# Performance work log

Hardware: AMD Instinct MI355X
Metric: run time of the kernel (lower is better)

## Reference

```python
import jax, jax.numpy as jnp
import numpy as np

U, I, D, E = 100000, 50000, 128, 3200000


def setup_inputs() -> dict:
    key = jax.random.key(0)
    k0, k1, k2, k3, k4 = jax.random.split(key, 5)
    stdv = 1.0 / np.sqrt(D)
    return {
        "user_embedding": jax.random.uniform(k0, (U, D), jnp.float32, -stdv, stdv),
        "item_embedding": jax.random.uniform(k1, (I, D), jnp.float32, -stdv, stdv),
        "edge_vals": jax.random.uniform(k2, (E,), jnp.float32),  # normalized adj values
        "edge_u": jax.random.randint(k3, (E,), 0, U, jnp.int32),
        "edge_i": jax.random.randint(k4, (E,), 0, I, jnp.int32),
        "n_layers": 3,
    }


def reference(user_embedding, item_embedding, edge_vals, edge_u, edge_i, n_layers):
    # LightGCN forward: alternate SpMM on bipartite graph G [U,I] (COO edges),
    # then average embeddings across layers 0..n_layers.
    num_users = user_embedding.shape[0]
    num_items = item_embedding.shape[0]
    u_list = [user_embedding]
    i_list = [item_embedding]
    w = edge_vals[:, None]  # [E,1]
    for layer in range(n_layers):
        # u_{l+1} = G @ i_l : gather item rows along edges, scale, scatter-add to users
        new_u = jax.ops.segment_sum(w * i_list[layer][edge_i], edge_u,
                                    num_segments=num_users)
        # i_{l+1} = G^T @ u_l
        new_i = jax.ops.segment_sum(w * u_list[layer][edge_u], edge_i,
                                    num_segments=num_items)
        u_list.append(new_u)
        i_list.append(new_i)
    denom = jnp.float32(n_layers + 1)
    embed_user = sum(u_list) / denom
    embed_item = sum(i_list) / denom
    return (embed_user, embed_item)
```

## Files before the change

### kernel.cpp

```cpp
#include <hip/hip_runtime.h>


#define D 128
#define CHUNK 16384
#define SRCMASK 0x3FFFF
#define TPB 256

__device__ inline unsigned pack4(float a, float b, float c, float d, float qs) {
    int q0 = __float2int_rn(a * qs), q1 = __float2int_rn(b * qs);
    int q2 = __float2int_rn(c * qs), q3 = __float2int_rn(d * qs);
    return ((unsigned)(q0 & 255)) | ((unsigned)(q1 & 255) << 8) |
           ((unsigned)(q2 & 255) << 16) | ((unsigned)(q3 & 255) << 24);
}

__device__ inline void acc_q8(float4& sa, float4& sb, uint2 raw, float m) {
    unsigned x = raw.x, y = raw.y;
    sa.x += m * (float)((int)(x << 24) >> 24);
    sa.y += m * (float)((int)(x << 16) >> 24);
    sa.z += m * (float)((int)(x <<  8) >> 24);
    sa.w += m * (float)((int)(x      ) >> 24);
    sb.x += m * (float)((int)(y << 24) >> 24);
    sb.y += m * (float)((int)(y << 16) >> 24);
    sb.z += m * (float)((int)(y <<  8) >> 24);
    sb.w += m * (float)((int)(y      ) >> 24);
}

__global__ __launch_bounds__(TPB) void k_quant8(
    const float* __restrict__ ue, const float* __restrict__ ie,
    uint2* __restrict__ h0q, float* __restrict__ sc0, int U, int UA, int NP) {
    int row = blockIdx.x * (TPB / 16) + (threadIdx.x >> 4);
    if (row >= NP) return;
    int lane = threadIdx.x & 15;
    float4 a = make_float4(0.f, 0.f, 0.f, 0.f);
    float4 b = make_float4(0.f, 0.f, 0.f, 0.f);
    const float* p = nullptr;
    if (row < U)        p = ue + (size_t)row * D + lane * 8;
    else if (row >= UA) p = ie + (size_t)(row - UA) * D + lane * 8;
    if (p) { a = *(const float4*)p; b = *(const float4*)(p + 4); }
    float m = fmaxf(fmaxf(fmaxf(fabsf(a.x), fabsf(a.y)), fmaxf(fabsf(a.z), fabsf(a.w))),
                    fmaxf(fmaxf(fabsf(b.x), fabsf(b.y)), fmaxf(fabsf(b.z), fabsf(b.w))));
    for (int d_ = 1; d_ < 16; d_ <<= 1) m = fmaxf(m, __shfl_xor(m, d_));
    float qs = (m > 0.f) ? 127.f / m : 0.f;
    uint2 q;
    q.x = pack4(a.x, a.y, a.z, a.w, qs);
    q.y = pack4(b.x, b.y, b.z, b.w, qs);
    h0q[(size_t)row * 16 + lane] = q;
    if (lane == 0) sc0[row] = m * (1.f / 127.f);
}

__global__ __launch_bounds__(256) void k_count(const int* __restrict__ eu,
                                               const int* __restrict__ ei,
                                               int* __restrict__ C, int E, int NB, int UA) {
    extern __shared__ int hist[];
    for (int k = threadIdx.x; k < NB; k += blockDim.x) hist[k] = 0;
    __syncthreads();
    int base = blockIdx.x * CHUNK;
    int n = min(CHUNK, E - base);
    for (int t = threadIdx.x; t < n; t += blockDim.x) {
        int u = eu[base + t];
        int i = ei[base + t];
        atomicAdd(&hist[u >> 6], 1);
        atomicAdd(&hist[(UA + i) >> 6], 1);
    }
    __syncthreads();
    int* Crow = C + (size_t)blockIdx.x * NB;
    for (int k = threadIdx.x; k < NB; k += blockDim.x) Crow[k] = hist[k];
}

__global__ void k_btot(const int* __restrict__ C, int* __restrict__ T, int NB, int NC) {
    int b = blockIdx.x * blockDim.x + threadIdx.x;
    if (b >= NB) return;
    int s = 0;
    for (int c = 0; c < NC; ++c) s += C[(size_t)c * NB + b];
    T[b] = s;
}

__global__ __launch_bounds__(1024) void k_scan(const int* __restrict__ T,
                                               int* __restrict__ offb, int N) {
    __shared__ int partial[1024];
    int t = threadIdx.x;
    int CH = (N + 1023) >> 10;
    int c0 = min(t * CH, N), c1 = min(c0 + CH, N);
    int sum = 0;
    for (int k = c0; k < c1; ++k) sum += T[k];
    partial[t] = sum;
    __syncthreads();
    for (int s = 1; s < 1024; s <<= 1) {
        int add = (t >= s) ? partial[t - s] : 0;
        __syncthreads();
        partial[t] += add;
        __syncthreads();
    }
    int run = (t == 0) ? 0 : partial[t - 1];
    for (int k = c0; k < c1; ++k) { offb[k] = run; run += T[k]; }
    if (t == 0) offb[N] = partial[1023];
}

__global__ void k_colscan(const int* __restrict__ C, const int* __restrict__ offb,
                          int* __restrict__ colScan, int NB, int NC) {
    int b = blockIdx.x * blockDim.x + threadIdx.x;
    if (b >= NB) return;
    int run = offb[b];
    for (int c = 0; c < NC; ++c) {
        size_t k = (size_t)c * NB + b;
        colScan[k] = run;
        run += C[k];
    }
}

__global__ __launch_bounds__(256) void k_cscatter(
    const int* __restrict__ eu, const int* __restrict__ ei, const float* __restrict__ w,
    const int* __restrict__ colScan, uint2* __restrict__ entA, int E, int NB, int UA) {
    extern __shared__ int cursor[];
    int c = blockIdx.x, t = threadIdx.x;
    const int* cs = colScan + (size_t)c * NB;
    for (int k = t; k < NB; k += 256) cursor[k] = cs[k];
    __syncthreads();
    int base = c * CHUNK;
    int n = min(CHUNK, E - base);
    for (int k = t; k < n; k += 256) {
        int u = eu[base + k];
        int gi = UA + ei[base + k];
        unsigned wb = __float_as_uint(w[base + k]);
        int pA = atomicAdd(&cursor[u >> 6], 1);
        entA[pA] = make_uint2(((unsigned)(u & 63) << 18) | (unsigned)gi, wb);
        int pB = atomicAdd(&cursor[gi >> 6], 1);
        entA[pB] = make_uint2(((unsigned)(gi & 63) << 18) | (unsigned)u, wb);
    }
}

__global__ __launch_bounds__(256) void k_rowsort(
    const uint2* __restrict__ entA, uint2* __restrict__ entB,
    const int* __restrict__ offb, int* __restrict__ off, int NP) {
    __shared__ int hist[64];
    __shared__ int rowOff[64];
    __shared__ int cursor[64];
    int b = blockIdx.x, t = threadIdx.x;
    int segBase = offb[b];
    int len = offb[b + 1] - segBase;
    if (t < 64) hist[t] = 0;
    __syncthreads();
    for (int k = t; k < len; k += 256)
        atomicAdd(&hist[entA[segBase + k].x >> 18], 1);
    __syncthreads();
    if (t == 0) {
        int run = 0;
        for (int r = 0; r < 64; ++r) { rowOff[r] = run; cursor[r] = run; run += hist[r]; }
    }
    __syncthreads();
    for (int k = t; k < len; k += 256) {
        uint2 e = entA[segBase + k];
        int p = atomicAdd(&cursor[e.x >> 18], 1);
        entB[segBase + p] = e;
    }
    if (t < 64) {
        int g = b * 64 + t;
        if (g <= NP) off[g] = segBase + rowOff[t];
    }
}

template <int MODE>
__global__ __launch_bounds__(TPB) void k_spmm(
    const uint2* __restrict__ q, const float* __restrict__ sc,
    uint2* __restrict__ nxtq, float* __restrict__ scn,
    const uint2* __restrict__ e1q, const float* __restrict__ sc1,
    const uint2* __restrict__ e2q, const float* __restrict__ sc2,
    const float* __restrict__ ue, const float* __restrict__ ie,
    float* __restrict__ out,
    const int* __restrict__ off, const uint2* __restrict__ csr,
    int U, int UA, int NP) {
    int row = blockIdx.x * (TPB / 16) + (threadIdx.x >> 4);
    if (row >= NP) return;
    int lane = threadIdx.x & 15;
    int beg = off[row], end = off[row + 1];
    float4 sa = make_float4(0.f, 0.f, 0.f, 0.f);
    float4 sb = make_float4(0.f, 0.f, 0.f, 0.f);

    int nIter = (end - beg) >> 2;
    int p = beg;
    if (nIter > 0) {
        uint2 m0 = csr[p], m1 = csr[p + 1], m2 = csr[p + 2], m3 = csr[p + 3];
        for (int it = 0; it < nIter; ++it) {
            int s0 = m0.x & SRCMASK, s1 = m1.x & SRCMASK;
            int s2 = m2.x & SRCMASK, s3 = m3.x & SRCMASK;
            uint2 g0 = q[(size_t)s0 * 16 + lane];
            uint2 g1 = q[(size_t)s1 * 16 + lane];
            uint2 g2 = q[(size_t)s2 * 16 + lane];
            uint2 g3 = q[(size_t)s3 * 16 + lane];
            float f0 = __uint_as_float(m0.y) * sc[s0];
            float f1 = __uint_as_float(m1.y) * sc[s1];
            float f2 = __uint_as_float(m2.y) * sc[s2];
            float f3 = __uint_as_float(m3.y) * sc[s3];
            int pn = p + 4;
            if (it + 1 < nIter) {
                m0 = csr[pn]; m1 = csr[pn + 1]; m2 = csr[pn + 2]; m3 = csr[pn + 3];
            }
            acc_q8(sa, sb, g0, f0);
            acc_q8(sa, sb, g1, f1);
            acc_q8(sa, sb, g2, f2);
            acc_q8(sa, sb, g3, f3);
            p = pn;
        }
    }
    for (; p < end; ++p) {
        uint2 m_ = csr[p];
        int s_ = m_.x & SRCMASK;
        uint2 g_ = q[(size_t)s_ * 16 + lane];
        acc_q8(sa, sb, g_, __uint_as_float(m_.y) * sc[s_]);
    }

    if (MODE == 0) {
        float m = fmaxf(fmaxf(fmaxf(fabsf(sa.x), fabsf(sa.y)), fmaxf(fabsf(sa.z), fabsf(sa.w))),
                        fmaxf(fmaxf(fabsf(sb.x), fabsf(sb.y)), fmaxf(fabsf(sb.z), fabsf(sb.w))));
        for (int d_ = 1; d_ < 16; d_ <<= 1) m = fmaxf(m, __shfl_xor(m, d_));
        float qs = (m > 0.f) ? 127.f / m : 0.f;
        uint2 qo;
        qo.x = pack4(sa.x, sa.y, sa.z, sa.w, qs);
        qo.y = pack4(sb.x, sb.y, sb.z, sb.w, qs);
        nxtq[(size_t)row * 16 + lane] = qo;
        if (lane == 0) scn[row] = m * (1.f / 127.f);
    } else {
        int outRow;
        const float* e0p;
        if (row < U)        { outRow = row;            e0p = ue + (size_t)row * D + lane * 8; }
        else if (row >= UA) { outRow = U + (row - UA); e0p = ie + (size_t)(row - UA) * D + lane * 8; }
        else return;
        float4 e0a = *(const float4*)e0p;
        float4 e0b = *(const float4*)(e0p + 4);
        uint2 q1 = e1q[(size_t)row * 16 + lane]; float s1r = sc1[row];
        uint2 q2 = e2q[(size_t)row * 16 + lane]; float s2r = sc2[row];
        unsigned x1 = q1.x, y1 = q1.y, x2 = q2.x, y2 = q2.y;
        float4 ra, rb;
        ra.x = 0.25f * (e0a.x + s1r * (float)((int)(x1 << 24) >> 24) + s2r * (float)((int)(x2 << 24) >> 24) + sa.x);
        ra.y = 0.25f * (e0a.y + s1r * (float)((int)(x1 << 16) >> 24) + s2r * (float)((int)(x2 << 16) >> 24) + sa.y);
        ra.z = 0.25f * (e0a.z + s1r * (float)((int)(x1 <<  8) >> 24) + s2r * (float)((int)(x2 <<  8) >> 24) + sa.z);
        ra.w = 0.25f * (e0a.w + s1r * (float)((int)(x1      ) >> 24) + s2r * (float)((int)(x2      ) >> 24) + sa.w);
        rb.x = 0.25f * (e0b.x + s1r * (float)((int)(y1 << 24) >> 24) + s2r * (float)((int)(y2 << 24) >> 24) + sb.x);
        rb.y = 0.25f * (e0b.y + s1r * (float)((int)(y1 << 16) >> 24) + s2r * (float)((int)(y2 << 16) >> 24) + sb.y);
        rb.z = 0.25f * (e0b.z + s1r * (float)((int)(y1 <<  8) >> 24) + s2r * (float)((int)(y2 <<  8) >> 24) + sb.z);
        rb.w = 0.25f * (e0b.w + s1r * (float)((int)(y1      ) >> 24) + s2r * (float)((int)(y2      ) >> 24) + sb.w);
        float* op = out + (size_t)outRow * D + lane * 8;
        *(float4*)op = ra;
        *(float4*)(op + 4) = rb;
    }
}

extern "C" void kernel_launch(void* const* d_in, const int* in_sizes, int n_in,
                              void* d_out, int out_size, void* d_ws, size_t ws_size,
                              hipStream_t stream) {
    const float* ue = (const float*)d_in[0];
    const float* ie = (const float*)d_in[1];
    const float* w  = (const float*)d_in[2];
    const int*   eu = (const int*)d_in[3];
    const int*   ei = (const int*)d_in[4];

    const int U  = in_sizes[0] / D;
    const int I  = in_sizes[1] / D;
    const int E  = in_sizes[2];
    const int UA = ((U + 63) >> 6) << 6;
    const int NP = UA + I;
    const int NB = (NP + 63) >> 6;
    const int NC = (E + CHUNK - 1) / CHUNK;
    const size_t nE2 = (size_t)2 * E;

    uint2* h0q = (uint2*)d_ws;
    uint2* e1q = h0q + (size_t)NP * 16;
    uint2* e2q = e1q + (size_t)NP * 16;
    float* sc0 = (float*)(e2q + (size_t)NP * 16);
    float* sc1 = sc0 + NP;
    float* sc2 = sc1 + NP;
    uint2* entB = (uint2*)(sc2 + NP);
    int* C       = (int*)(entB + nE2);
    int* colScan = C + (size_t)NC * NB;
    int* T       = colScan + (size_t)NC * NB;
    int* offb    = T + NB;
    int* off     = offb + NB + 1;
    char* tail   = (char*)(off + NP + 1);
    tail += (8 - ((uintptr_t)tail & 7)) & 7;
    uint2* entA  = (uint2*)tail;

    const size_t needed = (size_t)NP * D * 3 + (size_t)NP * 12
                        + nE2 * 8 * 2
                        + ((size_t)2 * NC * NB + NB + (NB + 1) + (NP + 1)) * 4 + 8;
    if (ws_size < needed) return;

    const int nbR = (NP + 15) / 16;

    k_quant8<<<nbR, TPB, 0, stream>>>(ue, ie, h0q, sc0, U, UA, NP);
    k_count<<<NC, 256, (size_t)NB * 4, stream>>>(eu, ei, C, E, NB, UA);
    k_btot<<<(NB + 255) / 256, 256, 0, stream>>>(C, T, NB, NC);
    k_scan<<<1, 1024, 0, stream>>>(T, offb, NB);
    k_colscan<<<(NB + 255) / 256, 256, 0, stream>>>(C, offb, colScan, NB, NC);
    k_cscatter<<<NC, 256, (size_t)NB * 4, stream>>>(eu, ei, w, colScan, entA, E, NB, UA);
    k_rowsort<<<NB, 256, 0, stream>>>(entA, entB, offb, off, NP);

    k_spmm<0><<<nbR, TPB, 0, stream>>>(h0q, sc0, e1q, sc1,
                                       nullptr, nullptr, nullptr, nullptr,
                                       ue, ie, nullptr, off, entB, U, UA, NP);
    k_spmm<0><<<nbR, TPB, 0, stream>>>(e1q, sc1, e2q, sc2,
                                       nullptr, nullptr, nullptr, nullptr,
                                       ue, ie, nullptr, off, entB, U, UA, NP);
    k_spmm<1><<<nbR, TPB, 0, stream>>>(e2q, sc2, nullptr, nullptr,
                                       e1q, sc1, e2q, sc2,
                                       ue, ie, (float*)d_out, off, entB, U, UA, NP);
}
```

Baseline: 646.4 us.

## Tile column scans, shrink edge chunks, widen blocks, and use nontemporal memory ops

The edge chunk size drops from 16384 to 4096, giving more blocks for counting and scatter. The serial per-bucket column sum and column scan are replaced by a two-level tiled scan (k_tile_sum, k_super, then a tiled colscan) so that work spreads over a 2D grid. The preprocessing kernels move to 512 threads per block, and many loads and stores across all kernels become nontemporal to avoid polluting the cache. The risks are a larger histogram matrix (four times the chunks, so C and colScan each grow fourfold) and possible cache-policy penalties on data that is reused, such as csr entries in the later SpMM layers.

```diff
diff --git a/kernel.cpp b/kernel.cpp
--- a/kernel.cpp
+++ b/kernel.cpp
@@ -2,9 +2,32 @@
 
 
 #define D 128
-#define CHUNK 16384
+#define CHUNK 4096
+#define CTILE 64
 #define SRCMASK 0x3FFFF
 #define TPB 256
+
+typedef unsigned int u32x2 __attribute__((ext_vector_type(2)));
+typedef float f32x4 __attribute__((ext_vector_type(4)));
+
+__device__ inline uint2 ntload_u2(const uint2* p) {
+    u32x2 v = __builtin_nontemporal_load((const u32x2*)p);
+    uint2 r; r.x = v.x; r.y = v.y; return r;
+}
+__device__ inline void ntstore_u2(uint2* p, uint2 v) {
+    u32x2 t; t.x = v.x; t.y = v.y;
+    __builtin_nontemporal_store(t, (u32x2*)p);
+}
+__device__ inline void ntstore_f4(float* p, float4 v) {
+    f32x4 t; t.x = v.x; t.y = v.y; t.z = v.z; t.w = v.w;
+    __builtin_nontemporal_store(t, (f32x4*)p);
+}
+__device__ inline int ntload_i(const int* p) { return __builtin_nontemporal_load(p); }
+__device__ inline float ntload_f(const float* p) { return __builtin_nontemporal_load(p); }
+__device__ inline float4 ntload_f4(const float* p) {
+    f32x4 v = __builtin_nontemporal_load((const f32x4*)p);
+    return make_float4(v.x, v.y, v.z, v.w);
+}
 
 __device__ inline unsigned pack4(float a, float b, float c, float d, float qs) {
     int q0 = __float2int_rn(a * qs), q1 = __float2int_rn(b * qs);
@@ -36,7 +59,7 @@
     const float* p = nullptr;
     if (row < U)        p = ue + (size_t)row * D + lane * 8;
     else if (row >= UA) p = ie + (size_t)(row - UA) * D + lane * 8;
-    if (p) { a = *(const float4*)p; b = *(const float4*)(p + 4); }
+    if (p) { a = ntload_f4(p); b = ntload_f4(p + 4); }
     float m = fmaxf(fmaxf(fmaxf(fabsf(a.x), fabsf(a.y)), fmaxf(fabsf(a.z), fabsf(a.w))),
                     fmaxf(fmaxf(fabsf(b.x), fabsf(b.y)), fmaxf(fabsf(b.z), fabsf(b.w))));
     for (int d_ = 1; d_ < 16; d_ <<= 1) m = fmaxf(m, __shfl_xor(m, d_));
@@ -48,7 +71,7 @@
     if (lane == 0) sc0[row] = m * (1.f / 127.f);
 }
 
-__global__ __launch_bounds__(256) void k_count(const int* __restrict__ eu,
+__global__ __launch_bounds__(512) void k_count(const int* __restrict__ eu,
                                                const int* __restrict__ ei,
                                                int* __restrict__ C, int E, int NB, int UA) {
     extern __shared__ int hist[];
@@ -57,22 +80,40 @@
     int base = blockIdx.x * CHUNK;
     int n = min(CHUNK, E - base);
     for (int t = threadIdx.x; t < n; t += blockDim.x) {
-        int u = eu[base + t];
-        int i = ei[base + t];
+        int u = ntload_i(eu + base + t);
+        int i = ntload_i(ei + base + t);
         atomicAdd(&hist[u >> 6], 1);
         atomicAdd(&hist[(UA + i) >> 6], 1);
     }
     __syncthreads();
     int* Crow = C + (size_t)blockIdx.x * NB;
-    for (int k = threadIdx.x; k < NB; k += blockDim.x) Crow[k] = hist[k];
-}
-
-__global__ void k_btot(const int* __restrict__ C, int* __restrict__ T, int NB, int NC) {
-    int b = blockIdx.x * blockDim.x + threadIdx.x;
+    for (int k = threadIdx.x; k < NB; k += blockDim.x)
+        __builtin_nontemporal_store(hist[k], Crow + k);
+}
+
+__global__ __launch_bounds__(256) void k_tile_sum(const int* __restrict__ C,
+                                                  int* __restrict__ S, int NB, int NC) {
+    int b = blockIdx.x * 256 + threadIdx.x;
     if (b >= NB) return;
+    int tc = blockIdx.y;
+    int c0 = tc * CTILE, c1 = min(c0 + CTILE, NC);
     int s = 0;
-    for (int c = 0; c < NC; ++c) s += C[(size_t)c * NB + b];
-    T[b] = s;
+    for (int c = c0; c < c1; ++c) s += C[(size_t)c * NB + b];
+    S[(size_t)tc * NB + b] = s;
+}
+
+__global__ __launch_bounds__(256) void k_super(int* __restrict__ S, int* __restrict__ T,
+                                               int NB, int TC) {
+    int b = blockIdx.x * 256 + threadIdx.x;
+    if (b >= NB) return;
+    int run = 0;
+    for (int tc = 0; tc < TC; ++tc) {
+        size_t k = (size_t)tc * NB + b;
+        int v = S[k];
+        S[k] = run;
+        run += v;
+    }
+    T[b] = run;
 }
 
 __global__ __launch_bounds__(1024) void k_scan(const int* __restrict__ T,
@@ -96,40 +137,44 @@
     if (t == 0) offb[N] = partial[1023];
 }
 
-__global__ void k_colscan(const int* __restrict__ C, const int* __restrict__ offb,
-                          int* __restrict__ colScan, int NB, int NC) {
-    int b = blockIdx.x * blockDim.x + threadIdx.x;
+__global__ __launch_bounds__(256) void k_colscan(const int* __restrict__ C,
+                                                 const int* __restrict__ S,
+                                                 const int* __restrict__ offb,
+                                                 int* __restrict__ colScan, int NB, int NC) {
+    int b = blockIdx.x * 256 + threadIdx.x;
     if (b >= NB) return;
-    int run = offb[b];
-    for (int c = 0; c < NC; ++c) {
+    int tc = blockIdx.y;
+    int c0 = tc * CTILE, c1 = min(c0 + CTILE, NC);
+    int run = offb[b] + S[(size_t)tc * NB + b];
+    for (int c = c0; c < c1; ++c) {
         size_t k = (size_t)c * NB + b;
-        colScan[k] = run;
+        __builtin_nontemporal_store(run, colScan + k);
         run += C[k];
     }
 }
 
-__global__ __launch_bounds__(256) void k_cscatter(
+__global__ __launch_bounds__(512) void k_cscatter(
     const int* __restrict__ eu, const int* __restrict__ ei, const float* __restrict__ w,
     const int* __restrict__ colScan, uint2* __restrict__ entA, int E, int NB, int UA) {
     extern __shared__ int cursor[];
     int c = blockIdx.x, t = threadIdx.x;
     const int* cs = colScan + (size_t)c * NB;
-    for (int k = t; k < NB; k += 256) cursor[k] = cs[k];
+    for (int k = t; k < NB; k += blockDim.x) cursor[k] = cs[k];
     __syncthreads();
     int base = c * CHUNK;
     int n = min(CHUNK, E - base);
-    for (int k = t; k < n; k += 256) {
-        int u = eu[base + k];
-        int gi = UA + ei[base + k];
-        unsigned wb = __float_as_uint(w[base + k]);
+    for (int k = t; k < n; k += blockDim.x) {
+        int u = ntload_i(eu + base + k);
+        int gi = UA + ntload_i(ei + base + k);
+        unsigned wb = __float_as_uint(ntload_f(w + base + k));
         int pA = atomicAdd(&cursor[u >> 6], 1);
-        entA[pA] = make_uint2(((unsigned)(u & 63) << 18) | (unsigned)gi, wb);
+        ntstore_u2(entA + pA, make_uint2(((unsigned)(u & 63) << 18) | (unsigned)gi, wb));
         int pB = atomicAdd(&cursor[gi >> 6], 1);
-        entA[pB] = make_uint2(((unsigned)(gi & 63) << 18) | (unsigned)u, wb);
-    }
-}
-
-__global__ __launch_bounds__(256) void k_rowsort(
+        ntstore_u2(entA + pB, make_uint2(((unsigned)(gi & 63) << 18) | (unsigned)u, wb));
+    }
+}
+
+__global__ __launch_bounds__(512) void k_rowsort(
     const uint2* __restrict__ entA, uint2* __restrict__ entB,
     const int* __restrict__ offb, int* __restrict__ off, int NP) {
     __shared__ int hist[64];
@@ -140,18 +185,20 @@
     int len = offb[b + 1] - segBase;
     if (t < 64) hist[t] = 0;
     __syncthreads();
-    for (int k = t; k < len; k += 256)
-        atomicAdd(&hist[entA[segBase + k].x >> 18], 1);
+    for (int k = t; k < len; k += blockDim.x) {
+        unsigned x = __builtin_nontemporal_load(&((const unsigned*)(entA + segBase + k))[0]);
+        atomicAdd(&hist[x >> 18], 1);
+    }
     __syncthreads();
     if (t == 0) {
         int run = 0;
         for (int r = 0; r < 64; ++r) { rowOff[r] = run; cursor[r] = run; run += hist[r]; }
     }
     __syncthreads();
-    for (int k = t; k < len; k += 256) {
-        uint2 e = entA[segBase + k];
+    for (int k = t; k < len; k += blockDim.x) {
+        uint2 e = ntload_u2(entA + segBase + k);
         int p = atomicAdd(&cursor[e.x >> 18], 1);
-        entB[segBase + p] = e;
+        ntstore_u2(entB + segBase + p, e);
     }
     if (t < 64) {
         int g = b * 64 + t;
@@ -172,14 +219,15 @@
     int row = blockIdx.x * (TPB / 16) + (threadIdx.x >> 4);
     if (row >= NP) return;
     int lane = threadIdx.x & 15;
-    int beg = off[row], end = off[row + 1];
+    int beg = ntload_i(off + row), end = ntload_i(off + row + 1);
     float4 sa = make_float4(0.f, 0.f, 0.f, 0.f);
     float4 sb = make_float4(0.f, 0.f, 0.f, 0.f);
 
     int nIter = (end - beg) >> 2;
     int p = beg;
     if (nIter > 0) {
-        uint2 m0 = csr[p], m1 = csr[p + 1], m2 = csr[p + 2], m3 = csr[p + 3];
+        uint2 m0 = ntload_u2(csr + p), m1 = ntload_u2(csr + p + 1);
+        uint2 m2 = ntload_u2(csr + p + 2), m3 = ntload_u2(csr + p + 3);
         for (int it = 0; it < nIter; ++it) {
             int s0 = m0.x & SRCMASK, s1 = m1.x & SRCMASK;
             int s2 = m2.x & SRCMASK, s3 = m3.x & SRCMASK;
@@ -193,7 +241,8 @@
             float f3 = __uint_as_float(m3.y) * sc[s3];
             int pn = p + 4;
             if (it + 1 < nIter) {
-                m0 = csr[pn]; m1 = csr[pn + 1]; m2 = csr[pn + 2]; m3 = csr[pn + 3];
+                m0 = ntload_u2(csr + pn);     m1 = ntload_u2(csr + pn + 1);
+                m2 = ntload_u2(csr + pn + 2); m3 = ntload_u2(csr + pn + 3);
             }
             acc_q8(sa, sb, g0, f0);
             acc_q8(sa, sb, g1, f1);
@@ -203,7 +252,7 @@
         }
     }
     for (; p < end; ++p) {
-        uint2 m_ = csr[p];
+        uint2 m_ = ntload_u2(csr + p);
         int s_ = m_.x & SRCMASK;
         uint2 g_ = q[(size_t)s_ * 16 + lane];
         acc_q8(sa, sb, g_, __uint_as_float(m_.y) * sc[s_]);
@@ -225,8 +274,8 @@
         if (row < U)        { outRow = row;            e0p = ue + (size_t)row * D + lane * 8; }
         else if (row >= UA) { outRow = U + (row - UA); e0p = ie + (size_t)(row - UA) * D + lane * 8; }
         else return;
-        float4 e0a = *(const float4*)e0p;
-        float4 e0b = *(const float4*)(e0p + 4);
+        float4 e0a = ntload_f4(e0p);
+        float4 e0b = ntload_f4(e0p + 4);
         uint2 q1 = e1q[(size_t)row * 16 + lane]; float s1r = sc1[row];
         uint2 q2 = e2q[(size_t)row * 16 + lane]; float s2r = sc2[row];
         unsigned x1 = q1.x, y1 = q1.y, x2 = q2.x, y2 = q2.y;
@@ -240,8 +289,8 @@
         rb.z = 0.25f * (e0b.z + s1r * (float)((int)(y1 <<  8) >> 24) + s2r * (float)((int)(y2 <<  8) >> 24) + sb.z);
         rb.w = 0.25f * (e0b.w + s1r * (float)((int)(y1      ) >> 24) + s2r * (float)((int)(y2      ) >> 24) + sb.w);
         float* op = out + (size_t)outRow * D + lane * 8;
-        *(float4*)op = ra;
-        *(float4*)(op + 4) = rb;
+        ntstore_f4(op, ra);
+        ntstore_f4(op + 4, rb);
     }
 }
 
@@ -261,6 +310,7 @@
     const int NP = UA + I;
     const int NB = (NP + 63) >> 6;
     const int NC = (E + CHUNK - 1) / CHUNK;
+    const int TC = (NC + CTILE - 1) / CTILE;
     const size_t nE2 = (size_t)2 * E;
 
     uint2* h0q = (uint2*)d_ws;
@@ -272,7 +322,8 @@
     uint2* entB = (uint2*)(sc2 + NP);
     int* C       = (int*)(entB + nE2);
     int* colScan = C + (size_t)NC * NB;
-    int* T       = colScan + (size_t)NC * NB;
+    int* S       = colScan + (size_t)NC * NB;
+    int* T       = S + (size_t)TC * NB;
     int* offb    = T + NB;
     int* off     = offb + NB + 1;
     char* tail   = (char*)(off + NP + 1);
@@ -281,18 +332,20 @@
 
     const size_t needed = (size_t)NP * D * 3 + (size_t)NP * 12
                         + nE2 * 8 * 2
-                        + ((size_t)2 * NC * NB + NB + (NB + 1) + (NP + 1)) * 4 + 8;
+                        + ((size_t)2 * NC * NB + (size_t)TC * NB + NB + (NB + 1) + (NP + 1)) * 4 + 8;
     if (ws_size < needed) return;
 
     const int nbR = (NP + 15) / 16;
+    const int TB = (NB + 255) / 256;
 
     k_quant8<<<nbR, TPB, 0, stream>>>(ue, ie, h0q, sc0, U, UA, NP);
-    k_count<<<NC, 256, (size_t)NB * 4, stream>>>(eu, ei, C, E, NB, UA);
-    k_btot<<<(NB + 255) / 256, 256, 0, stream>>>(C, T, NB, NC);
+    k_count<<<NC, 512, (size_t)NB * 4, stream>>>(eu, ei, C, E, NB, UA);
+    k_tile_sum<<<dim3(TB, TC), 256, 0, stream>>>(C, S, NB, NC);
+    k_super<<<TB, 256, 0, stream>>>(S, T, NB, TC);
     k_scan<<<1, 1024, 0, stream>>>(T, offb, NB);
-    k_colscan<<<(NB + 255) / 256, 256, 0, stream>>>(C, offb, colScan, NB, NC);
-    k_cscatter<<<NC, 256, (size_t)NB * 4, stream>>>(eu, ei, w, colScan, entA, E, NB, UA);
-    k_rowsort<<<NB, 256, 0, stream>>>(entA, entB, offb, off, NP);
+    k_colscan<<<dim3(TB, TC), 256, 0, stream>>>(C, S, offb, colScan, NB, NC);
+    k_cscatter<<<NC, 512, (size_t)NB * 4, stream>>>(eu, ei, w, colScan, entA, E, NB, UA);
+    k_rowsort<<<NB, 512, 0, stream>>>(entA, entB, offb, off, NP);
 
     k_spmm<0><<<nbR, TPB, 0, stream>>>(h0q, sc0, e1q, sc1,
                                        nullptr, nullptr, nullptr, nullptr,
```

After: 985.8 us. +52.5%, slower.
